# Kernel optimization log

Hardware: AMD Instinct MI355X
Metric: run time of the kernel (lower is better)

The kernel has to match this reference:

```python
import jax, jax.numpy as jnp
import numpy as np
import math

EPS = 1e-08


def setup_inputs() -> dict:
    key = jax.random.key(0)
    ks = jax.random.split(key, 5)
    N, n, d = 8, 32768, 128
    K, h, d_hat = 64, 128, 128
    return {
        "X": jax.random.normal(ks[0], (N, n, d), dtype=jnp.float32),
        "S": jax.random.normal(ks[1], (N, K, h), dtype=jnp.float32),
        "Wk": jax.random.normal(ks[2], (d, d_hat), dtype=jnp.float32) * (1.0 / math.sqrt(d)),
        "Wq": jax.random.normal(ks[3], (h, d_hat), dtype=jnp.float32) * (1.0 / math.sqrt(h)),
        "Wv": jax.random.normal(ks[4], (d, d_hat), dtype=jnp.float32) * (1.0 / math.sqrt(d)),
    }


def reference(X, S, Wk, Wq, Wv):
    # X: [N, n, d], S: [N, K, h]
    d_hat = Wk.shape[1]
    scale = 1.0 / math.sqrt(d_hat)
    k = jnp.einsum('bnd,de->bne', X, Wk)   # [N, n, d_hat]
    v = jnp.einsum('bnd,de->bne', X, Wv)   # [N, n, d_hat]
    q = jnp.einsum('bkh,he->bke', S, Wq)   # [N, K, d_hat]
    M = scale * jnp.einsum('bne,bke->bnk', k, q)  # [N, n, K]
    attn = jax.nn.sigmoid(M) + EPS
    W = attn / jnp.sum(attn, axis=2, keepdims=True)  # normalize over slots K
    S_hat = jnp.einsum('bnk,bne->bke', W, v)  # [N, K, d_hat]
    return S_hat
```

## Files before the change

### kernel.cpp

```cpp
#include <hip/hip_runtime.h>
#include <hip/hip_bf16.h>

typedef __attribute__((ext_vector_type(8))) short short8;
typedef __attribute__((ext_vector_type(4))) float f32x4;

#define N_BATCH 8
#define N_ROWS 32768
#define DDIM 128
#define KSLOT 64
#define EH 128
#define TPB 8
#define BLK_PER_B 64
#define SCALE 0.08838834764831845f

__device__ inline unsigned short f2bf(float f){
  unsigned int u = __builtin_bit_cast(unsigned int, f);
  u = (u + 0x7FFFu + ((u >> 16) & 1u)) >> 16;
  return (unsigned short)u;
}

__device__ inline unsigned int pk2bf(float lo, float hi){
  __hip_bfloat162 h = __float22bfloat162_rn(float2{lo, hi});
  unsigned int u;
  __builtin_memcpy(&u, &h, 4);
  return u;
}

__device__ inline void lds_barrier(){
  asm volatile("s_waitcnt lgkmcnt(0)" ::: "memory");
  __builtin_amdgcn_s_barrier();
}

__global__ void prep_qk_kernel(const float* __restrict__ S, const float* __restrict__ Wq,
                               const float* __restrict__ Wk, unsigned short* __restrict__ qk){
  int bs = blockIdx.x;
  __shared__ float srow[128];
  __shared__ float qrow[128];
  int t = threadIdx.x;
  srow[t] = S[bs * 128 + t];
  __syncthreads();
  float acc = 0.f;
  #pragma unroll 8
  for(int h = 0; h < 128; ++h) acc += srow[h] * Wq[h * 128 + t];
  qrow[t] = acc;
  __syncthreads();
  float acc2 = 0.f;
  #pragma unroll 8
  for(int e = 0; e < 128; ++e) acc2 += qrow[e] * Wk[t * 128 + e];
  qk[bs * 128 + t] = f2bf(acc2 * SCALE);
}

__global__ __launch_bounds__(256, 2) void sse_main_kernel(
    const float* __restrict__ X, const unsigned short* __restrict__ qkg,
    float* __restrict__ partials)
{
  __shared__ unsigned short qs[64][136];
  __shared__ unsigned short Xs[64][136];
  __shared__ unsigned short Xt[128][70];
  __shared__ unsigned short WTs[64][72];

  const int tid  = threadIdx.x;
  const int wave = tid >> 6;
  const int lane = tid & 63;
  const int l15  = lane & 15;
  const int g    = lane >> 4;
  const int l31  = lane & 31;
  const int half = lane >> 5;

  const int b  = blockIdx.x / BLK_PER_B;
  const int tb = blockIdx.x % BLK_PER_B;

  const float* Xb = X + (size_t)b * N_ROWS * DDIM;
  const unsigned short* qkb = qkg + b * KSLOT * EH;

  #pragma unroll
  for(int i = 0; i < 4; ++i){
    int o = (i * 256 + tid) * 8;
    *reinterpret_cast<short8*>(&qs[o >> 7][o & 127]) =
        *reinterpret_cast<const short8*>(qkb + o);
  }

  f32x4 sacc[8];
  #pragma unroll
  for(int i = 0; i < 8; ++i) sacc[i] = {0.f, 0.f, 0.f, 0.f};

  const float* xw = Xb + (size_t)(tb * TPB * 64 + wave * 16) * DDIM + lane * 4;

  f32x4 xa[8];
  #pragma unroll
  for(int c = 0; c < 8; ++c)
    xa[c] = *reinterpret_cast<const f32x4*>(xw + c * 256);

  lds_barrier();

  const int wr0 = wave * 16;

  #pragma unroll
  for(int tt = 0; tt < TPB; ++tt){

    #pragma unroll
    for(int m = 0; m < 4; ++m){
      const int nb = wr0 + 4 * m;
      unsigned int p0a = pk2bf(xa[2*m][0],   xa[2*m][1]);
      unsigned int p0b = pk2bf(xa[2*m][2],   xa[2*m][3]);
      unsigned int p1a = pk2bf(xa[2*m+1][0], xa[2*m+1][1]);
      unsigned int p1b = pk2bf(xa[2*m+1][2], xa[2*m+1][3]);
      uint2 s0; s0.x = p0a; s0.y = p0b;
      uint2 s1; s1.x = p1a; s1.y = p1b;
      *reinterpret_cast<uint2*>(&Xs[nb + half][4 * l31])     = s0;
      *reinterpret_cast<uint2*>(&Xs[nb + 2 + half][4 * l31]) = s1;
      unsigned int q0a = (unsigned int)__shfl_xor((int)p0a, 32);
      unsigned int q0b = (unsigned int)__shfl_xor((int)p0b, 32);
      unsigned int q1a = (unsigned int)__shfl_xor((int)p1a, 32);
      unsigned int q1b = (unsigned int)__shfl_xor((int)p1b, 32);
      unsigned int A = half ? q0b : p0a;
      unsigned int B = half ? p0b : q0a;
      unsigned int C = half ? q1b : p1a;
      unsigned int D = half ? p1b : q1a;
      const int d0 = 4 * l31 + 2 * half;
      unsigned int wlo0 = __builtin_amdgcn_perm(B, A, 0x05040100u);
      unsigned int wlo1 = __builtin_amdgcn_perm(D, C, 0x05040100u);
      unsigned int whi0 = __builtin_amdgcn_perm(B, A, 0x07060302u);
      unsigned int whi1 = __builtin_amdgcn_perm(D, C, 0x07060302u);
      *reinterpret_cast<unsigned int*>(&Xt[d0][nb])         = wlo0;
      *reinterpret_cast<unsigned int*>(&Xt[d0][nb + 2])     = wlo1;
      *reinterpret_cast<unsigned int*>(&Xt[d0 + 1][nb])     = whi0;
      *reinterpret_cast<unsigned int*>(&Xt[d0 + 1][nb + 2]) = whi1;
    }

    if(tt + 1 < TPB){
      const float* xp = xw + (size_t)(tt + 1) * 64 * DDIM;
      #pragma unroll
      for(int c = 0; c < 8; ++c)
        xa[c] = *reinterpret_cast<const f32x4*>(xp + c * 256);
    }

    f32x4 macc[4];
    #pragma unroll
    for(int i = 0; i < 4; ++i) macc[i] = {0.f,0.f,0.f,0.f};
    __builtin_amdgcn_s_setprio(1);
    #pragma unroll
    for(int step = 0; step < 4; ++step){
      short8 a = *reinterpret_cast<const short8*>(&Xs[wr0 + l15][step * 32 + g * 8]);
      #pragma unroll
      for(int st = 0; st < 4; ++st){
        short8 bq = *reinterpret_cast<const short8*>(&qs[st * 16 + l15][step * 32 + g * 8]);
        macc[st] = __builtin_amdgcn_mfma_f32_16x16x32_bf16(a, bq, macc[st], 0, 0, 0);
      }
    }
    __builtin_amdgcn_s_setprio(0);

    float att[4][4];
    float rinv[4];
    #pragma unroll
    for(int st = 0; st < 4; ++st){
      #pragma unroll
      for(int r = 0; r < 4; ++r)
        att[st][r] = __builtin_amdgcn_rcpf(1.f + __expf(-macc[st][r])) + 1e-8f;
    }
    #pragma unroll
    for(int r = 0; r < 4; ++r){
      float s = att[0][r] + att[1][r] + att[2][r] + att[3][r];
      s += __shfl_xor(s, 1); s += __shfl_xor(s, 2);
      s += __shfl_xor(s, 4); s += __shfl_xor(s, 8);
      rinv[r] = __builtin_amdgcn_rcpf(s);
    }
    #pragma unroll
    for(int st = 0; st < 4; ++st){
      unsigned int u0 = pk2bf(att[st][0] * rinv[0], att[st][1] * rinv[1]);
      unsigned int u1 = pk2bf(att[st][2] * rinv[2], att[st][3] * rinv[3]);
      ushort4 wp;
      __builtin_memcpy(&wp, &u0, 4);
      __builtin_memcpy(reinterpret_cast<char*>(&wp) + 4, &u1, 4);
      *reinterpret_cast<ushort4*>(&WTs[st * 16 + l15][wave * 16 + g * 4]) = wp;
    }
    lds_barrier();

    __builtin_amdgcn_s_setprio(1);
    #pragma unroll
    for(int ns = 0; ns < 2; ++ns){
      short8 af = *reinterpret_cast<const short8*>(&WTs[wr0 + l15][ns * 32 + g * 8]);
      #pragma unroll
      for(int et = 0; et < 8; ++et){
        short8 bf = *reinterpret_cast<const short8*>(&Xt[et * 16 + l15][ns * 32 + g * 8]);
        sacc[et] = __builtin_amdgcn_mfma_f32_16x16x32_bf16(af, bf, sacc[et], 0, 0, 0);
      }
    }
    __builtin_amdgcn_s_setprio(0);
    lds_barrier();
  }

  float* po = partials + (size_t)blockIdx.x * (KSLOT * EH);
  #pragma unroll
  for(int et = 0; et < 8; ++et){
    #pragma unroll
    for(int r = 0; r < 4; ++r)
      po[(wave * 16 + g * 4 + r) * EH + et * 16 + l15] = sacc[et][r];
  }
}

__global__ void reduce_kernel(const float* __restrict__ partials,
                              const float* __restrict__ Wv, float* __restrict__ out){
  int bs = blockIdx.x;
  int b  = bs >> 6;
  int s  = bs & 63;
  __shared__ float Tl[128];
  int t = threadIdx.x;
  const float* pb = partials + (size_t)b * BLK_PER_B * (KSLOT * EH) + s * EH + t;
  float acc = 0.f;
  #pragma unroll 8
  for(int i = 0; i < BLK_PER_B; ++i)
    acc += pb[(size_t)i * (KSLOT * EH)];
  Tl[t] = acc;
  __syncthreads();
  float o = 0.f;
  #pragma unroll 8
  for(int d = 0; d < 128; ++d) o += Tl[d] * Wv[d * 128 + t];
  out[bs * 128 + t] = o;
}

extern "C" void kernel_launch(void* const* d_in, const int* in_sizes, int n_in,
                              void* d_out, int out_size, void* d_ws, size_t ws_size,
                              hipStream_t stream){
  const float* X  = (const float*)d_in[0];
  const float* S  = (const float*)d_in[1];
  const float* Wk = (const float*)d_in[2];
  const float* Wq = (const float*)d_in[3];
  const float* Wv = (const float*)d_in[4];
  float* out = (float*)d_out;

  char* ws = (char*)d_ws;
  unsigned short* qk = (unsigned short*)(ws);
  float* partials    = (float*)(ws + 131072);

  hipLaunchKernelGGL(prep_qk_kernel, dim3(512), dim3(128), 0, stream, S, Wq, Wk, qk);
  hipLaunchKernelGGL(sse_main_kernel, dim3(N_BATCH * BLK_PER_B), dim3(256), 0, stream,
                     X, qk, partials);
  hipLaunchKernelGGL(reduce_kernel, dim3(512), dim3(128), 0, stream, partials, Wv, out);
}
```

Measured before the change: 55.11 us.

## Hold qk fragments in registers and double-buffer Xt/WTs to drop a barrier

The prep kernel now writes the scaled q·Wk^T matrix pre-swizzled into MFMA fragment order, so each wave loads its 16 B-operand fragments straight into registers instead of staging them in LDS. Xt and WTs are double-buffered by iteration parity, which removes the trailing LDS barrier per iteration. Launch bounds drop to one block per SM, which allows more registers for the held fragments but may reduce occupancy. The Xs buffer stays single while its trailing barrier is gone, which could let the next iteration's writes race with reads still in progress.

```diff
diff --git a/kernel.cpp b/kernel.cpp
--- a/kernel.cpp
+++ b/kernel.cpp
@@ -32,10 +32,11 @@
 }
 
 __global__ void prep_qk_kernel(const float* __restrict__ S, const float* __restrict__ Wq,
-                               const float* __restrict__ Wk, unsigned short* __restrict__ qk){
+                               const float* __restrict__ Wk, unsigned short* __restrict__ qf){
   int bs = blockIdx.x;
   __shared__ float srow[128];
   __shared__ float qrow[128];
+  __shared__ float krow[128];
   int t = threadIdx.x;
   srow[t] = S[bs * 128 + t];
   __syncthreads();
@@ -47,17 +48,27 @@
   float acc2 = 0.f;
   #pragma unroll 8
   for(int e = 0; e < 128; ++e) acc2 += qrow[e] * Wk[t * 128 + e];
-  qk[bs * 128 + t] = f2bf(acc2 * SCALE);
-}
-
-__global__ __launch_bounds__(256, 2) void sse_main_kernel(
-    const float* __restrict__ X, const unsigned short* __restrict__ qkg,
+  krow[t] = acc2 * SCALE;
+  __syncthreads();
+  if(t < 16){
+    int step = t >> 2, g = t & 3;
+    int b = bs >> 6, s = bs & 63;
+    int st = s >> 4, l15 = s & 15;
+    short8 v;
+    #pragma unroll
+    for(int e = 0; e < 8; ++e) v[e] = (short)f2bf(krow[step * 32 + g * 8 + e]);
+    *reinterpret_cast<short8*>(qf + (size_t)b * 8192 +
+        (size_t)(((st * 4 + step) * 64 + g * 16 + l15) * 8)) = v;
+  }
+}
+
+__global__ __launch_bounds__(256, 1) void sse_main_kernel(
+    const float* __restrict__ X, const unsigned short* __restrict__ qf,
     float* __restrict__ partials)
 {
-  __shared__ unsigned short qs[64][136];
   __shared__ unsigned short Xs[64][136];
-  __shared__ unsigned short Xt[128][70];
-  __shared__ unsigned short WTs[64][72];
+  __shared__ unsigned short Xt[2][128][70];
+  __shared__ unsigned short WTs[2][64][72];
 
   const int tid  = threadIdx.x;
   const int wave = tid >> 6;
@@ -71,14 +82,15 @@
   const int tb = blockIdx.x % BLK_PER_B;
 
   const float* Xb = X + (size_t)b * N_ROWS * DDIM;
-  const unsigned short* qkb = qkg + b * KSLOT * EH;
-
-  #pragma unroll
-  for(int i = 0; i < 4; ++i){
-    int o = (i * 256 + tid) * 8;
-    *reinterpret_cast<short8*>(&qs[o >> 7][o & 127]) =
-        *reinterpret_cast<const short8*>(qkb + o);
-  }
+  const unsigned short* qkb = qf + (size_t)b * 8192;
+
+  short8 bq[4][4];
+  #pragma unroll
+  for(int st = 0; st < 4; ++st)
+    #pragma unroll
+    for(int step = 0; step < 4; ++step)
+      bq[st][step] = *reinterpret_cast<const short8*>(qkb +
+          (size_t)(((st * 4 + step) * 64 + lane) * 8));
 
   f32x4 sacc[8];
   #pragma unroll
@@ -91,12 +103,11 @@
   for(int c = 0; c < 8; ++c)
     xa[c] = *reinterpret_cast<const f32x4*>(xw + c * 256);
 
-  lds_barrier();
-
   const int wr0 = wave * 16;
 
   #pragma unroll
   for(int tt = 0; tt < TPB; ++tt){
+    const int buf = tt & 1;
 
     #pragma unroll
     for(int m = 0; m < 4; ++m){
@@ -122,10 +133,10 @@
       unsigned int wlo1 = __builtin_amdgcn_perm(D, C, 0x05040100u);
       unsigned int whi0 = __builtin_amdgcn_perm(B, A, 0x07060302u);
       unsigned int whi1 = __builtin_amdgcn_perm(D, C, 0x07060302u);
-      *reinterpret_cast<unsigned int*>(&Xt[d0][nb])         = wlo0;
-      *reinterpret_cast<unsigned int*>(&Xt[d0][nb + 2])     = wlo1;
-      *reinterpret_cast<unsigned int*>(&Xt[d0 + 1][nb])     = whi0;
-      *reinterpret_cast<unsigned int*>(&Xt[d0 + 1][nb + 2]) = whi1;
+      *reinterpret_cast<unsigned int*>(&Xt[buf][d0][nb])         = wlo0;
+      *reinterpret_cast<unsigned int*>(&Xt[buf][d0][nb + 2])     = wlo1;
+      *reinterpret_cast<unsigned int*>(&Xt[buf][d0 + 1][nb])     = whi0;
+      *reinterpret_cast<unsigned int*>(&Xt[buf][d0 + 1][nb + 2]) = whi1;
     }
 
     if(tt + 1 < TPB){
@@ -143,10 +154,8 @@
     for(int step = 0; step < 4; ++step){
       short8 a = *reinterpret_cast<const short8*>(&Xs[wr0 + l15][step * 32 + g * 8]);
       #pragma unroll
-      for(int st = 0; st < 4; ++st){
-        short8 bq = *reinterpret_cast<const short8*>(&qs[st * 16 + l15][step * 32 + g * 8]);
-        macc[st] = __builtin_amdgcn_mfma_f32_16x16x32_bf16(a, bq, macc[st], 0, 0, 0);
-      }
+      for(int st = 0; st < 4; ++st)
+        macc[st] = __builtin_amdgcn_mfma_f32_16x16x32_bf16(a, bq[st][step], macc[st], 0, 0, 0);
     }
     __builtin_amdgcn_s_setprio(0);
 
@@ -172,22 +181,22 @@
       ushort4 wp;
       __builtin_memcpy(&wp, &u0, 4);
       __builtin_memcpy(reinterpret_cast<char*>(&wp) + 4, &u1, 4);
-      *reinterpret_cast<ushort4*>(&WTs[st * 16 + l15][wave * 16 + g * 4]) = wp;
-    }
+      *reinterpret_cast<ushort4*>(&WTs[buf][st * 16 + l15][wave * 16 + g * 4]) = wp;
+    }
+
     lds_barrier();
 
     __builtin_amdgcn_s_setprio(1);
     #pragma unroll
     for(int ns = 0; ns < 2; ++ns){
-      short8 af = *reinterpret_cast<const short8*>(&WTs[wr0 + l15][ns * 32 + g * 8]);
+      short8 af = *reinterpret_cast<const short8*>(&WTs[buf][wr0 + l15][ns * 32 + g * 8]);
       #pragma unroll
       for(int et = 0; et < 8; ++et){
-        short8 bf = *reinterpret_cast<const short8*>(&Xt[et * 16 + l15][ns * 32 + g * 8]);
+        short8 bf = *reinterpret_cast<const short8*>(&Xt[buf][et * 16 + l15][ns * 32 + g * 8]);
         sacc[et] = __builtin_amdgcn_mfma_f32_16x16x32_bf16(af, bf, sacc[et], 0, 0, 0);
       }
     }
     __builtin_amdgcn_s_setprio(0);
-    lds_barrier();
   }
 
   float* po = partials + (size_t)blockIdx.x * (KSLOT * EH);
@@ -230,11 +239,11 @@
   float* out = (float*)d_out;
 
   char* ws = (char*)d_ws;
-  unsigned short* qk = (unsigned short*)(ws);
+  unsigned short* qf = (unsigned short*)(ws);
   float* partials    = (float*)(ws + 131072);
 
-  hipLaunchKernelGGL(prep_qk_kernel, dim3(512), dim3(128), 0, stream, S, Wq, Wk, qk);
+  hipLaunchKernelGGL(prep_qk_kernel, dim3(512), dim3(128), 0, stream, S, Wq, Wk, qf);
   hipLaunchKernelGGL(sse_main_kernel, dim3(N_BATCH * BLK_PER_B), dim3(256), 0, stream,
-                     X, qk, partials);
+                     X, qf, partials);
   hipLaunchKernelGGL(reduce_kernel, dim3(512), dim3(128), 0, stream, partials, Wv, out);
 }
```

After: 52.90 us. 4.0% less time.

## Keep attention weights in registers and accumulate per-wave slot partials

Applied to the files above, without the earlier changes.

The second GEMM (W^T·X) no longer stages the normalized attention weights through shared memory. Each wave now uses its own MFMA output fragments directly as A operands of 16x16x16 bf16 MFMAs over its 16 rows. Each wave also gets a private transposed X tile, which removes both intra-loop block barriers. The cost is that each wave holds a full 64x128 accumulator (128 VGPRs), so occupancy drops to one block per CU. A cross-wave reduction through LDS is added at the end, along with more, smaller-K MFMA instructions.

```diff
diff --git a/kernel.cpp b/kernel.cpp
--- a/kernel.cpp
+++ b/kernel.cpp
@@ -2,6 +2,7 @@
 #include <hip/hip_bf16.h>
 
 typedef __attribute__((ext_vector_type(8))) short short8;
+typedef __attribute__((ext_vector_type(4))) short short4v;
 typedef __attribute__((ext_vector_type(4))) float f32x4;
 
 #define N_BATCH 8
@@ -50,14 +51,14 @@
   qk[bs * 128 + t] = f2bf(acc2 * SCALE);
 }
 
-__global__ __launch_bounds__(256, 2) void sse_main_kernel(
+__global__ __launch_bounds__(256, 1) void sse_main_kernel(
     const float* __restrict__ X, const unsigned short* __restrict__ qkg,
     float* __restrict__ partials)
 {
-  __shared__ unsigned short qs[64][136];
-  __shared__ unsigned short Xs[64][136];
-  __shared__ unsigned short Xt[128][70];
-  __shared__ unsigned short WTs[64][72];
+  __shared__ char smem[55296];
+  unsigned short (*qs)[136]  = (unsigned short(*)[136])(smem);
+  unsigned short (*Xs)[136]  = (unsigned short(*)[136])(smem + 17408);
+  unsigned short (*Xtw)[20]  = (unsigned short(*)[20]) (smem + 34816);
 
   const int tid  = threadIdx.x;
   const int wave = tid >> 6;
@@ -80,9 +81,11 @@
         *reinterpret_cast<const short8*>(qkb + o);
   }
 
-  f32x4 sacc[8];
-  #pragma unroll
-  for(int i = 0; i < 8; ++i) sacc[i] = {0.f, 0.f, 0.f, 0.f};
+  f32x4 sacc[4][8];
+  #pragma unroll
+  for(int i = 0; i < 4; ++i)
+    #pragma unroll
+    for(int j = 0; j < 8; ++j) sacc[i][j] = {0.f, 0.f, 0.f, 0.f};
 
   const float* xw = Xb + (size_t)(tb * TPB * 64 + wave * 16) * DDIM + lane * 4;
 
@@ -94,6 +97,7 @@
   lds_barrier();
 
   const int wr0 = wave * 16;
+  unsigned short (*xtw)[20] = &Xtw[wave * 128];
 
   #pragma unroll
   for(int tt = 0; tt < TPB; ++tt){
@@ -122,10 +126,10 @@
       unsigned int wlo1 = __builtin_amdgcn_perm(D, C, 0x05040100u);
       unsigned int whi0 = __builtin_amdgcn_perm(B, A, 0x07060302u);
       unsigned int whi1 = __builtin_amdgcn_perm(D, C, 0x07060302u);
-      *reinterpret_cast<unsigned int*>(&Xt[d0][nb])         = wlo0;
-      *reinterpret_cast<unsigned int*>(&Xt[d0][nb + 2])     = wlo1;
-      *reinterpret_cast<unsigned int*>(&Xt[d0 + 1][nb])     = whi0;
-      *reinterpret_cast<unsigned int*>(&Xt[d0 + 1][nb + 2]) = whi1;
+      uint2 wv0; wv0.x = wlo0; wv0.y = wlo1;
+      uint2 wv1; wv1.x = whi0; wv1.y = whi1;
+      *reinterpret_cast<uint2*>(&xtw[d0][4 * m])     = wv0;
+      *reinterpret_cast<uint2*>(&xtw[d0 + 1][4 * m]) = wv1;
     }
 
     if(tt + 1 < TPB){
@@ -165,37 +169,56 @@
       s += __shfl_xor(s, 4); s += __shfl_xor(s, 8);
       rinv[r] = __builtin_amdgcn_rcpf(s);
     }
+    short4v wfrag[4];
     #pragma unroll
     for(int st = 0; st < 4; ++st){
       unsigned int u0 = pk2bf(att[st][0] * rinv[0], att[st][1] * rinv[1]);
       unsigned int u1 = pk2bf(att[st][2] * rinv[2], att[st][3] * rinv[3]);
-      ushort4 wp;
-      __builtin_memcpy(&wp, &u0, 4);
-      __builtin_memcpy(reinterpret_cast<char*>(&wp) + 4, &u1, 4);
-      *reinterpret_cast<ushort4*>(&WTs[st * 16 + l15][wave * 16 + g * 4]) = wp;
-    }
+      short4v wf;
+      __builtin_memcpy(&wf, &u0, 4);
+      __builtin_memcpy(reinterpret_cast<char*>(&wf) + 4, &u1, 4);
+      wfrag[st] = wf;
+    }
+
+    __builtin_amdgcn_s_setprio(1);
+    #pragma unroll
+    for(int et = 0; et < 8; ++et){
+      short4v xt = *reinterpret_cast<const short4v*>(&xtw[et * 16 + l15][4 * g]);
+#if __has_builtin(__builtin_amdgcn_mfma_f32_16x16x16bf16_1k)
+      #pragma unroll
+      for(int sta = 0; sta < 4; ++sta)
+        sacc[sta][et] = __builtin_amdgcn_mfma_f32_16x16x16bf16_1k(
+            wfrag[sta], xt, sacc[sta][et], 0, 0, 0);
+#else
+      short8 b8 = {xt[0], xt[1], xt[2], xt[3], 0, 0, 0, 0};
+      #pragma unroll
+      for(int sta = 0; sta < 4; ++sta){
+        short8 a8 = {wfrag[sta][0], wfrag[sta][1], wfrag[sta][2], wfrag[sta][3], 0, 0, 0, 0};
+        sacc[sta][et] = __builtin_amdgcn_mfma_f32_16x16x32_bf16(a8, b8, sacc[sta][et], 0, 0, 0);
+      }
+#endif
+    }
+    __builtin_amdgcn_s_setprio(0);
+  }
+
+  lds_barrier();
+  float* stg = (float*)smem;
+  float* po = partials + (size_t)blockIdx.x * (KSLOT * EH);
+  #pragma unroll
+  for(int sta = 0; sta < 4; ++sta){
+    #pragma unroll
+    for(int et = 0; et < 8; ++et)
+      #pragma unroll
+      for(int r = 0; r < 4; ++r)
+        stg[wave * 2048 + (g * 4 + r) * 128 + et * 16 + l15] = sacc[sta][et][r];
     lds_barrier();
-
-    __builtin_amdgcn_s_setprio(1);
-    #pragma unroll
-    for(int ns = 0; ns < 2; ++ns){
-      short8 af = *reinterpret_cast<const short8*>(&WTs[wr0 + l15][ns * 32 + g * 8]);
-      #pragma unroll
-      for(int et = 0; et < 8; ++et){
-        short8 bf = *reinterpret_cast<const short8*>(&Xt[et * 16 + l15][ns * 32 + g * 8]);
-        sacc[et] = __builtin_amdgcn_mfma_f32_16x16x32_bf16(af, bf, sacc[et], 0, 0, 0);
-      }
-    }
-    __builtin_amdgcn_s_setprio(0);
+    #pragma unroll
+    for(int k = 0; k < 8; ++k){
+      int idx = k * 256 + tid;
+      float v = stg[idx] + stg[2048 + idx] + stg[4096 + idx] + stg[6144 + idx];
+      po[sta * 2048 + idx] = v;
+    }
     lds_barrier();
-  }
-
-  float* po = partials + (size_t)blockIdx.x * (KSLOT * EH);
-  #pragma unroll
-  for(int et = 0; et < 8; ++et){
-    #pragma unroll
-    for(int r = 0; r < 4; ++r)
-      po[(wave * 16 + g * 4 + r) * EH + et * 16 + l15] = sacc[et][r];
   }
 }
 
```

Measured after the change: 52.01 us. -5.6%, faster.

## Halve rows per block, double grid, store bf16 partials via LDS staging

Applied to the files above, without the earlier changes.

Reduces tiles per block from 8 to 4 and doubles the number of blocks per batch to 128, giving 1024 blocks for better load balance across CUs. Per-block partial sums are now staged through LDS, packed to bf16 and written with 16-byte stores, and the reduce kernel converts them back to float. This keeps partial traffic near its previous size despite twice as many partials. The cost is precision lost by rounding partials to bf16 before the reduction, and the reduce kernel has a longer loop.

```diff
diff --git a/kernel.cpp b/kernel.cpp
--- a/kernel.cpp
+++ b/kernel.cpp
@@ -9,14 +9,18 @@
 #define DDIM 128
 #define KSLOT 64
 #define EH 128
-#define TPB 8
-#define BLK_PER_B 64
+#define TPB 4
+#define BLK_PER_B 128
 #define SCALE 0.08838834764831845f
 
 __device__ inline unsigned short f2bf(float f){
   unsigned int u = __builtin_bit_cast(unsigned int, f);
   u = (u + 0x7FFFu + ((u >> 16) & 1u)) >> 16;
   return (unsigned short)u;
+}
+__device__ inline float bf2f(unsigned short h){
+  unsigned int u = ((unsigned int)h) << 16;
+  return __builtin_bit_cast(float, u);
 }
 
 __device__ inline unsigned int pk2bf(float lo, float hi){
@@ -52,7 +56,7 @@
 
 __global__ __launch_bounds__(256, 2) void sse_main_kernel(
     const float* __restrict__ X, const unsigned short* __restrict__ qkg,
-    float* __restrict__ partials)
+    unsigned short* __restrict__ partials)
 {
   __shared__ unsigned short qs[64][136];
   __shared__ unsigned short Xs[64][136];
@@ -190,27 +194,48 @@
     lds_barrier();
   }
 
-  float* po = partials + (size_t)blockIdx.x * (KSLOT * EH);
-  #pragma unroll
-  for(int et = 0; et < 8; ++et){
-    #pragma unroll
-    for(int r = 0; r < 4; ++r)
-      po[(wave * 16 + g * 4 + r) * EH + et * 16 + l15] = sacc[et][r];
+  float* stgf = (float*)(&qs[0][0]);
+  unsigned short* po = partials + (size_t)blockIdx.x * (KSLOT * EH);
+  #pragma unroll
+  for(int rd = 0; rd < 2; ++rd){
+    #pragma unroll
+    for(int et = 0; et < 4; ++et){
+      const int ee = rd * 4 + et;
+      #pragma unroll
+      for(int r = 0; r < 4; ++r)
+        stgf[(wr0 + g * 4 + r) * 64 + et * 16 + l15] = sacc[ee][r];
+    }
+    lds_barrier();
+    {
+      int base = tid * 16;
+      int slot = base >> 6;
+      int d0   = base & 63;
+      union { short8 s; unsigned int u[4]; } pk0, pk1;
+      #pragma unroll
+      for(int j = 0; j < 4; ++j){
+        pk0.u[j] = pk2bf(stgf[base + 2*j],     stgf[base + 2*j + 1]);
+        pk1.u[j] = pk2bf(stgf[base + 8 + 2*j], stgf[base + 8 + 2*j + 1]);
+      }
+      unsigned short* dst = po + slot * 128 + rd * 64 + d0;
+      *reinterpret_cast<short8*>(dst)     = pk0.s;
+      *reinterpret_cast<short8*>(dst + 8) = pk1.s;
+    }
+    lds_barrier();
   }
 }
 
-__global__ void reduce_kernel(const float* __restrict__ partials,
+__global__ void reduce_kernel(const unsigned short* __restrict__ partials,
                               const float* __restrict__ Wv, float* __restrict__ out){
   int bs = blockIdx.x;
   int b  = bs >> 6;
   int s  = bs & 63;
   __shared__ float Tl[128];
   int t = threadIdx.x;
-  const float* pb = partials + (size_t)b * BLK_PER_B * (KSLOT * EH) + s * EH + t;
+  const unsigned short* pb = partials + (size_t)b * BLK_PER_B * (KSLOT * EH) + s * EH + t;
   float acc = 0.f;
   #pragma unroll 8
   for(int i = 0; i < BLK_PER_B; ++i)
-    acc += pb[(size_t)i * (KSLOT * EH)];
+    acc += bf2f(pb[(size_t)i * (KSLOT * EH)]);
   Tl[t] = acc;
   __syncthreads();
   float o = 0.f;
@@ -230,8 +255,8 @@
   float* out = (float*)d_out;
 
   char* ws = (char*)d_ws;
-  unsigned short* qk = (unsigned short*)(ws);
-  float* partials    = (float*)(ws + 131072);
+  unsigned short* qk       = (unsigned short*)(ws);
+  unsigned short* partials = (unsigned short*)(ws + 131072);
 
   hipLaunchKernelGGL(prep_qk_kernel, dim3(512), dim3(128), 0, stream, S, Wq, Wk, qk);
   hipLaunchKernelGGL(sse_main_kernel, dim3(N_BATCH * BLK_PER_B), dim3(256), 0, stream,
```

After: 59.42 us. +7.8%, slower.
